# Kernel optimization log

Hardware: AMD Instinct MI355X
Metric: run time of the kernel (lower is better)

## Reference

```python
import jax, jax.numpy as jnp
import numpy as np

B, S, H = 4, 2048, 3072
NQ, NKV, D = 16, 8, 256
NEG = -2.3819763e38  # large negative for masking


def setup_inputs() -> dict:
    key = jax.random.key(0)
    ks = jax.random.split(key, 8)
    hidden_states = jax.random.normal(ks[0], (B, S, H), dtype=jnp.float32)
    # rotary frequencies: angle theta per (pos, dim-pair), Gemma-style base 10000
    inv_freq = 1.0 / (10000.0 ** (np.arange(0, D, 2, dtype=np.float32) / D))  # [D/2]
    t = np.arange(S, dtype=np.float32)
    ang = np.outer(t, inv_freq)  # [S, D/2]
    freqs_cos = jnp.broadcast_to(jnp.asarray(np.cos(ang)), (B, S, D // 2)).astype(jnp.float32)
    freqs_sin = jnp.broadcast_to(jnp.asarray(np.sin(ang)), (B, S, D // 2)).astype(jnp.float32)
    # additive causal mask [B,1,S,S]
    causal = jnp.tril(jnp.ones((S, S), dtype=bool))
    mask = jnp.where(causal, 0.0, NEG).astype(jnp.float32)[None, None]
    mask = jnp.broadcast_to(mask, (B, 1, S, S))
    sc = 0.02
    wq = jax.random.normal(ks[1], (NQ * D, H), dtype=jnp.float32) * sc
    wk = jax.random.normal(ks[2], (NKV * D, H), dtype=jnp.float32) * sc
    wv = jax.random.normal(ks[3], (NKV * D, H), dtype=jnp.float32) * sc
    wo = jax.random.normal(ks[4], (H, NQ * D), dtype=jnp.float32) * sc
    return {"hidden_states": hidden_states, "freqs_cos": freqs_cos,
            "freqs_sin": freqs_sin, "mask": mask,
            "wq": wq, "wk": wk, "wv": wv, "wo": wo}


def _apply_rotary(x, cos, sin):
    # x: [B,S,N,Dh]; cos/sin: [B,S,Dh/2]. Complex rotation: (x1 + i x2) * (cos + i sin)
    d2 = x.shape[-1] // 2
    x1, x2 = x[..., :d2], x[..., d2:]
    c = cos[:, :, None, :]
    s = sin[:, :, None, :]
    return jnp.concatenate([x1 * c - x2 * s, x1 * s + x2 * c], axis=-1)


def reference(hidden_states, freqs_cos, freqs_sin, mask, wq, wk, wv, wo):
    b, s, _ = hidden_states.shape
    scaling = D ** -0.5
    xq = (hidden_states @ wq.T).reshape(b, s, NQ, D)
    xk = (hidden_states @ wk.T).reshape(b, s, NKV, D)
    xv = (hidden_states @ wv.T).reshape(b, s, NKV, D)
    xq = _apply_rotary(xq, freqs_cos, freqs_sin)
    xk = _apply_rotary(xk, freqs_cos, freqs_sin)
    # GQA: repeat kv heads to match query heads
    g = NQ // NKV
    xk = jnp.repeat(xk, g, axis=2)  # [b,s,NQ,D]
    xv = jnp.repeat(xv, g, axis=2)
    scores = jnp.einsum('bqhd,bkhd->bhqk', xq * scaling, xk) + mask
    probs = jax.nn.softmax(scores, axis=-1)
    out = jnp.einsum('bhqk,bkhd->bqhd', probs, xv).reshape(b, s, NQ * D)
    return out @ wo.T
```

## Files before the change

kernel.cpp:

```cpp
#include <hip/hip_runtime.h>

#define DEVI __device__ __forceinline__

typedef __attribute__((ext_vector_type(8))) short s16x8;
typedef __attribute__((ext_vector_type(4))) float f32x4;
typedef unsigned short u16;

DEVI u16 f2bf(float f){
  unsigned u = __float_as_uint(f);
  u += 0x7FFFu + ((u >> 16) & 1u);
  return (u16)(u >> 16);
}
DEVI float bf2f(u16 s){ return __uint_as_float(((unsigned)s) << 16); }

DEVI void gload16(const void* g, void* l){
  __builtin_amdgcn_global_load_lds((const __attribute__((address_space(1))) void*)g,
                                   (__attribute__((address_space(3))) void*)l, 16, 0, 0);
}

__global__ __launch_bounds__(256) void cast_bf16_kernel(const float* __restrict__ src,
                                                        u16* __restrict__ dst, int n4){
  int i = blockIdx.x*256 + threadIdx.x;
  if (i < n4){
    float4 v = reinterpret_cast<const float4*>(src)[i];
    ushort4 o;
    o.x = f2bf(v.x); o.y = f2bf(v.y); o.z = f2bf(v.z); o.w = f2bf(v.w);
    reinterpret_cast<ushort4*>(dst)[i] = o;
  }
}

template<int MODE>
__global__ __launch_bounds__(512,2) void gemm8p_kernel(
    const u16* __restrict__ A, const u16* __restrict__ Bw,
    int K, int nbn, int Nn,
    const float* __restrict__ fc, const float* __restrict__ fs,
    float* __restrict__ Cf, u16* __restrict__ Qo, u16* __restrict__ Ko, u16* __restrict__ Vo)
{
  __shared__ u16 LDSb[2][32768];
  const int nwg = gridDim.x;
  const int bid0 = blockIdx.x;
  const int bid = (bid0 & 7)*(nwg >> 3) + (bid0 >> 3);
  const int bm = bid / nbn, bn = bid % nbn;
  const int t = threadIdx.x, ln = t&63;
  const int wvid = t>>6;
  const int wr = wvid>>2, wc = wvid&3;
  const int frow = ln&15, g = ln>>4;
  const int NT = K >> 6;

  size_t soff[2];
  #pragma unroll
  for (int i=0;i<2;i++){
    const int phys = (i*512 + t)*16;
    const int L = phys ^ (((phys>>7)&7)<<4);
    soff[i] = (size_t)(L >> 7) * K + ((L & 127) >> 1);
  }
  const u16* Apan = A  + (size_t)(bm*256)*K;
  const u16* Bpan = Bw + (size_t)(bn*256)*K;

  int aoff[8][2], boff[4][2];
  #pragma unroll
  for (int mi=0;mi<8;mi++){
    const int row = mi*16 + frow;
    #pragma unroll
    for (int ks=0;ks<2;ks++){
      const int L = row*128 + ks*64 + g*16;
      aoff[mi][ks] = wr*16384 + (L ^ ((row&7)<<4));
    }
  }
  #pragma unroll
  for (int ni=0;ni<4;ni++){
    const int row128 = wc*32 + (ni&1)*16 + frow;
    const int half   = ni>>1;
    #pragma unroll
    for (int ks=0;ks<2;ks++){
      const int L = row128*128 + ks*64 + g*16;
      boff[ni][ks] = 32768 + half*16384 + (L ^ ((row128&7)<<4));
    }
  }

  f32x4 acc[8][4];
  #pragma unroll
  for (int i=0;i<8;i++)
    #pragma unroll
    for (int j=0;j<4;j++) acc[i][j] = f32x4{0.f,0.f,0.f,0.f};

  auto stageHalf = [&](int buf, int ht, int tstep){
    char* dst = (char*)&LDSb[buf][0] + ht*16384;
    const u16* src = (ht < 2 ? Apan : Bpan) + (size_t)((ht&1)*128)*K + (size_t)tstep*64;
    #pragma unroll
    for (int i=0;i<2;i++)
      gload16(src + soff[i], dst + (i*512 + t)*16);
  };

  stageHalf(0,0,0); stageHalf(0,1,0); stageHalf(0,2,0); stageHalf(0,3,0);
  if (NT > 1){ stageHalf(1,2,1); stageHalf(1,3,1); }
  asm volatile("s_waitcnt vmcnt(4)" ::: "memory");
  __builtin_amdgcn_s_barrier();

  for (int T=0; T<NT; ++T){
    const char* sb = (const char*)&LDSb[T&1][0];
    s16x8 bh[4][2];
    #pragma unroll
    for (int p=0;p<4;++p){
      if (p==0){
        #pragma unroll
        for (int ni=0;ni<4;ni++)
          #pragma unroll
          for (int ks=0;ks<2;ks++)
            bh[ni][ks] = *(const s16x8*)(sb + boff[ni][ks]);
      }
      s16x8 afr[2][2];
      #pragma unroll
      for (int m2=0;m2<2;m2++)
        #pragma unroll
        for (int ks=0;ks<2;ks++)
          afr[m2][ks] = *(const s16x8*)(sb + aoff[p*2+m2][ks]);
      if      (p==0){ if (T+1 < NT) stageHalf((T+1)&1, 0, T+1); }
      else if (p==1){ if (T+1 < NT) stageHalf((T+1)&1, 1, T+1); }
      else if (p==2){ if (T+2 < NT) stageHalf(T&1,     2, T+2); }
      else          { if (T+2 < NT) stageHalf(T&1,     3, T+2); }
      __builtin_amdgcn_s_barrier();
      asm volatile("s_waitcnt lgkmcnt(0)" ::: "memory");
      __builtin_amdgcn_sched_barrier(0);
      __builtin_amdgcn_s_setprio(1);
      #pragma unroll
      for (int ks=0;ks<2;ks++)
        #pragma unroll
        for (int m2=0;m2<2;m2++)
          #pragma unroll
          for (int ni=0;ni<4;ni++)
            acc[p*2+m2][ni] = __builtin_amdgcn_mfma_f32_16x16x32_bf16(
                afr[m2][ks], bh[ni][ks], acc[p*2+m2][ni], 0,0,0);
      __builtin_amdgcn_s_setprio(0);
      __builtin_amdgcn_sched_barrier(0);
      if (p==3){
        if (T+2 < NT)       { asm volatile("s_waitcnt vmcnt(4)" ::: "memory"); }
        else if (T+2 == NT) { asm volatile("s_waitcnt vmcnt(0)" ::: "memory"); }
      }
      __builtin_amdgcn_s_barrier();
    }
  }

  const int mbase = bm*256 + wr*128;
  if (MODE == 0 && bn < 24){
    const bool isQ = (bn < 16);
    u16* dstB = isQ ? Qo : Ko;
    const int h  = isQ ? bn : (bn - 16);
    const int NH = isQ ? 16 : 8;
    #pragma unroll
    for (int mi=0;mi<8;mi++){
      #pragma unroll
      for (int ni=0;ni<2;ni++){
        const int dd = wc*32 + ni*16 + frow;
        #pragma unroll
        for (int r=0;r<4;r++){
          const int m = mbase + mi*16 + g*4 + r;
          const int b = m >> 11, s = m & 2047;
          const size_t ci = ((size_t)(b*2048 + s))*128 + dd;
          const float c  = fc[ci];
          const float sn = fs[ci];
          const float x1 = acc[mi][ni][r], x2 = acc[mi][ni+2][r];
          const size_t base = (((size_t)(b*NH + h)*2048 + s) << 8);
          dstB[base + dd]       = f2bf(x1*c - x2*sn);
          dstB[base + dd + 128] = f2bf(x1*sn + x2*c);
        }
      }
    }
  } else if (MODE == 0){
    u16* TB = (u16*)&LDSb[0][0];
    const int h  = bn - 24;
    const int b  = (bm*256) >> 11;
    const int s0 = (bm*256) & 2047;
    #pragma unroll
    for (int mi=0;mi<8;mi++){
      #pragma unroll
      for (int ni=0;ni<4;ni++){
        const int d  = wc*32 + (ni>>1)*128 + (ni&1)*16 + frow;
        const int sl = wr*128 + mi*16 + g*4;
        alignas(8) u16 p4[4];
        #pragma unroll
        for (int r=0;r<4;r++) p4[r] = f2bf(acc[mi][ni][r]);
        const int Tphys = (d*512 + sl*2) ^ ((d&7)<<4);
        *(uint2*)((char*)TB + Tphys) = *(const uint2*)p4;
      }
    }
    __syncthreads();
    #pragma unroll
    for (int i=0;i<16;i++){
      const int ci = i*512 + t;
      const int d = ci >> 5, sb2 = (ci & 31)*16;
      const int phys = (d*512 + sb2) ^ ((d&7)<<4);
      const s16x8 val = *(const s16x8*)((const char*)TB + phys);
      *(s16x8*)&Vo[(((size_t)(b*8 + h)*256 + d)*2048) + s0 + (sb2>>1)] = val;
    }
  } else {
    #pragma unroll
    for (int mi=0;mi<8;mi++){
      #pragma unroll
      for (int ni=0;ni<4;ni++){
        const int n = bn*256 + wc*32 + (ni>>1)*128 + (ni&1)*16 + frow;
        #pragma unroll
        for (int r=0;r<4;r++){
          const int m = mbase + mi*16 + g*4 + r;
          Cf[(size_t)m*Nn + n] = acc[mi][ni][r];
        }
      }
    }
  }
}

__global__ __launch_bounds__(512,2) void flash_attn_kernel(
    const u16* __restrict__ Qg, const u16* __restrict__ Kg,
    const u16* __restrict__ VTg, u16* __restrict__ Og)
{
  __shared__ u16 Kl[2][32*256];
  __shared__ u16 Vt[2][256*32];
  __shared__ u16 Pl[8][16*40];
  const int xb = blockIdx.x;
  const int kvh = blockIdx.y, b = blockIdx.z;
  const int t = threadIdx.x, wvid = t>>6, ln = t&63;
  const int frow = ln&15, g = ln>>4;
  const int qh = kvh*2 + (wvid>>2);
  const u16* Qp = Qg  + ((size_t)(b*16 + qh) << 19);
  const u16* Kp = Kg  + ((size_t)(b*8 + kvh) << 19);
  const u16* Vp = VTg + ((size_t)(b*8 + kvh) << 19);

  s16x8 ones;
  #pragma unroll
  for (int j=0;j<8;j++) ones[j] = (short)0x3F80;

  int kge[2]; int vrow[2]; int vcb[2];
  #pragma unroll
  for (int i=0;i<2;i++){
    const int ci = i*512 + t;
    kge[i] = (ci*8) ^ ((((unsigned)ci>>5)&7)<<3);
    const int phys = ci*16;
    const int L = phys ^ (((phys>>6)&3)<<4);
    vrow[i] = L >> 6;  vcb[i] = (L & 63) >> 1;
  }

  auto stageKV = [&](int kbase, int buf){
    #pragma unroll
    for (int i=0;i<2;i++){
      const int ci = i*512 + t;
      gload16(Kp + (size_t)kbase*256 + kge[i], &Kl[buf][(ci & ~63)*8]);
    }
    #pragma unroll
    for (int i=0;i<2;i++){
      const int ci = i*512 + t;
      gload16(Vp + (size_t)vrow[i]*2048 + kbase + vcb[i], &Vt[buf][(ci & ~63)*8]);
    }
  };

  #pragma unroll 1
  for (int seg=0; seg<2; seg++){
    const int qb = seg ? (31 - xb) : xb;
    const int q0 = qb*64 + (wvid&3)*16;
    const int ntiles = qb*2 + 2;

    s16x8 aq[8];
    #pragma unroll
    for (int kk=0;kk<8;kk++){
      s16x8 v = *(const s16x8*)&Qp[(size_t)(q0+frow)*256 + kk*32 + g*8];
      #pragma unroll
      for (int j=0;j<8;j++) v[j] = (short)f2bf(bf2f((u16)v[j]) * 0.0625f);
      aq[kk] = v;
    }

    f32x4 accO[16];
    #pragma unroll
    for (int i=0;i<16;i++) accO[i] = f32x4{0.f,0.f,0.f,0.f};
    f32x4 accL = f32x4{0.f,0.f,0.f,0.f};

    stageKV(0, 0);
    __syncthreads();

    for (int kt=0; kt<ntiles; kt++){
      const int kbase = kt*32;
      if (kt+1 < ntiles) stageKV(kbase + 32, (kt+1)&1);

      if (kbase <= q0 + 15){
        const char* Kb8 = (const char*)&Kl[kt&1][0];
        f32x4 sc[2];
        sc[0] = f32x4{0.f,0.f,0.f,0.f};
        sc[1] = f32x4{0.f,0.f,0.f,0.f};
        #pragma unroll
        for (int kb=0;kb<2;kb++){
          const int rr = kb*16 + frow;
          const int sw = (rr&7)<<4;
          const int bb = rr*512 + g*16;
          #pragma unroll
          for (int kk=0;kk<8;kk++){
            const s16x8 bk = *(const s16x8*)(Kb8 + ((bb + kk*64) ^ sw));
            sc[kb] = __builtin_amdgcn_mfma_f32_16x16x32_bf16(aq[kk], bk, sc[kb], 0,0,0);
          }
        }
        if (kbase + 31 > q0){
          #pragma unroll
          for (int r=0;r<4;r++){
            const int qrow = q0 + g*4 + r;
            if (kbase + frow > qrow)      sc[0][r] = -1e30f;
            if (kbase + 16 + frow > qrow) sc[1][r] = -1e30f;
          }
        }
        #pragma unroll
        for (int r=0;r<4;r++){
          const float p0 = __expf(fminf(sc[0][r], 30.f) - 8.f);
          const float p1 = __expf(fminf(sc[1][r], 30.f) - 8.f);
          Pl[wvid][(g*4+r)*40 + frow]      = f2bf(p0);
          Pl[wvid][(g*4+r)*40 + 16 + frow] = f2bf(p1);
        }
        asm volatile("s_waitcnt lgkmcnt(0)" ::: "memory");
        __builtin_amdgcn_sched_barrier(0);
        const s16x8 pf = *(const s16x8*)&Pl[wvid][frow*40 + g*8];
        accL = __builtin_amdgcn_mfma_f32_16x16x32_bf16(pf, ones, accL, 0,0,0);
        const char* Vb8 = (const char*)&Vt[kt&1][0];
        #pragma unroll
        for (int nb=0;nb<16;nb++){
          const int row = nb*16 + frow;
          const s16x8 vf = *(const s16x8*)(Vb8 + ((row*64 + g*16) ^ ((row&3)<<4)));
          accO[nb] = __builtin_amdgcn_mfma_f32_16x16x32_bf16(pf, vf, accO[nb], 0,0,0);
        }
      }

      __syncthreads();
    }

    f32x4 rl;
    #pragma unroll
    for (int r=0;r<4;r++) rl[r] = 1.0f / accL[r];
    #pragma unroll
    for (int nb=0;nb<16;nb++)
      #pragma unroll
      for (int r=0;r<4;r++){
        const int qrow = q0 + g*4 + r;
        Og[(((size_t)(b*2048 + qrow)*16 + qh) << 8) + nb*16 + frow] = f2bf(accO[nb][r] * rl[r]);
      }
  }
}

extern "C" void kernel_launch(void* const* d_in, const int* in_sizes, int n_in,
                              void* d_out, int out_size, void* d_ws, size_t ws_size,
                              hipStream_t stream) {
  const float* hidden = (const float*)d_in[0];
  const float* fcos   = (const float*)d_in[1];
  const float* fsin   = (const float*)d_in[2];
  const float* wq = (const float*)d_in[4];
  const float* wk = (const float*)d_in[5];
  const float* wv = (const float*)d_in[6];
  const float* wo = (const float*)d_in[7];
  float* out = (float*)d_out;

  char* ws = (char*)d_ws;
  u16* Xb   = (u16*)(ws);
  u16* Wcat = (u16*)(ws + 50331648);
  u16* Wob  = (u16*)(ws + 100663296);
  u16* Qb   = (u16*)(ws + 125829120);
  u16* Kb   = (u16*)(ws + 192937984);
  u16* VTb  = (u16*)(ws + 226492416);
  u16* AOb  = (u16*)(ws + 260046848);

  cast_bf16_kernel<<<24576, 256, 0, stream>>>(hidden, Xb, 6291456);
  cast_bf16_kernel<<<12288, 256, 0, stream>>>(wq, Wcat,              3145728);
  cast_bf16_kernel<<< 6144, 256, 0, stream>>>(wk, Wcat + 12582912,   1572864);
  cast_bf16_kernel<<< 6144, 256, 0, stream>>>(wv, Wcat + 18874368,   1572864);
  cast_bf16_kernel<<<12288, 256, 0, stream>>>(wo, Wob,               3145728);

  gemm8p_kernel<0><<<32*32, 512, 0, stream>>>(Xb, Wcat, 3072, 32, 8192,
                                              fcos, fsin, nullptr, Qb, Kb, VTb);

  flash_attn_kernel<<<dim3(16,8,4), 512, 0, stream>>>(Qb, Kb, VTb, AOb);

  gemm8p_kernel<1><<<32*12, 512, 0, stream>>>(AOb, Wob, 4096, 12, 3072,
                                              nullptr, nullptr, out, nullptr, nullptr, nullptr);
}
```

Before: 937.1 us.

## Fuse weight/input casts into one kernel and halve M-tile for output GEMM

Replaces five separate fp32-to-bf16 cast launches with a single grid-stride kernel that routes each index to the right source and destination. It also templates the GEMM on the M tile size and runs the output projection with 128-row tiles instead of 256, doubling its workgroup count from 384 to 768. The smaller tile is meant to fill the GPU's compute units better on the small output GEMM, at the cost of lower per-workgroup reuse of B tiles. The QKV GEMM keeps the original tile.

```diff
diff --git a/kernel.cpp b/kernel.cpp
--- a/kernel.cpp
+++ b/kernel.cpp
@@ -18,25 +18,39 @@
                                    (__attribute__((address_space(3))) void*)l, 16, 0, 0);
 }
 
-__global__ __launch_bounds__(256) void cast_bf16_kernel(const float* __restrict__ src,
-                                                        u16* __restrict__ dst, int n4){
-  int i = blockIdx.x*256 + threadIdx.x;
-  if (i < n4){
-    float4 v = reinterpret_cast<const float4*>(src)[i];
+__global__ __launch_bounds__(256) void cast_all_kernel(
+    const float* __restrict__ h,  const float* __restrict__ wq,
+    const float* __restrict__ wk, const float* __restrict__ wv,
+    const float* __restrict__ wo,
+    u16* __restrict__ Xb, u16* __restrict__ Wcat, u16* __restrict__ Wob)
+{
+  const int total = 15728640;
+  for (int i = blockIdx.x*256 + threadIdx.x; i < total; i += gridDim.x*256){
+    const float* src; u16* dst; int off;
+    if (i < 6291456)      { src = h;  dst = Xb;              off = i; }
+    else if (i < 9437184) { src = wq; dst = Wcat;            off = i - 6291456; }
+    else if (i < 11010048){ src = wk; dst = Wcat + 12582912; off = i - 9437184; }
+    else if (i < 12582912){ src = wv; dst = Wcat + 18874368; off = i - 11010048; }
+    else                  { src = wo; dst = Wob;             off = i - 12582912; }
+    float4 v = reinterpret_cast<const float4*>(src)[off];
     ushort4 o;
     o.x = f2bf(v.x); o.y = f2bf(v.y); o.z = f2bf(v.z); o.w = f2bf(v.w);
-    reinterpret_cast<ushort4*>(dst)[i] = o;
-  }
-}
-
-template<int MODE>
+    reinterpret_cast<ushort4*>(dst)[off] = o;
+  }
+}
+
+template<int MODE, int MI>
 __global__ __launch_bounds__(512,2) void gemm8p_kernel(
     const u16* __restrict__ A, const u16* __restrict__ Bw,
     int K, int nbn, int Nn,
     const float* __restrict__ fc, const float* __restrict__ fs,
     float* __restrict__ Cf, u16* __restrict__ Qo, u16* __restrict__ Ko, u16* __restrict__ Vo)
 {
-  __shared__ u16 LDSb[2][32768];
+  constexpr int AH   = MI*2048;
+  constexpr int BOFF = 2*AH;
+  constexpr int ACH  = MI/4;
+  constexpr int APH  = MI/4;
+  __shared__ u16 LDSb[2][(BOFF + 32768)/2];
   const int nwg = gridDim.x;
   const int bid0 = blockIdx.x;
   const int bid = (bid0 & 7)*(nwg >> 3) + (bid0 >> 3);
@@ -47,24 +61,30 @@
   const int frow = ln&15, g = ln>>4;
   const int NT = K >> 6;
 
-  size_t soff[2];
+  size_t soffA[ACH], soffB[2];
+  #pragma unroll
+  for (int i=0;i<ACH;i++){
+    const int phys = (i*512 + t)*16;
+    const int L = phys ^ (((phys>>7)&7)<<4);
+    soffA[i] = (size_t)(L >> 7) * K + ((L & 127) >> 1);
+  }
   #pragma unroll
   for (int i=0;i<2;i++){
     const int phys = (i*512 + t)*16;
     const int L = phys ^ (((phys>>7)&7)<<4);
-    soff[i] = (size_t)(L >> 7) * K + ((L & 127) >> 1);
-  }
-  const u16* Apan = A  + (size_t)(bm*256)*K;
+    soffB[i] = (size_t)(L >> 7) * K + ((L & 127) >> 1);
+  }
+  const u16* Apan = A  + (size_t)(bm*(MI*32))*K;
   const u16* Bpan = Bw + (size_t)(bn*256)*K;
 
-  int aoff[8][2], boff[4][2];
-  #pragma unroll
-  for (int mi=0;mi<8;mi++){
+  int aoff[MI][2], boff[4][2];
+  #pragma unroll
+  for (int mi=0;mi<MI;mi++){
     const int row = mi*16 + frow;
     #pragma unroll
     for (int ks=0;ks<2;ks++){
       const int L = row*128 + ks*64 + g*16;
-      aoff[mi][ks] = wr*16384 + (L ^ ((row&7)<<4));
+      aoff[mi][ks] = wr*AH + (L ^ ((row&7)<<4));
     }
   }
   #pragma unroll
@@ -74,22 +94,30 @@
     #pragma unroll
     for (int ks=0;ks<2;ks++){
       const int L = row128*128 + ks*64 + g*16;
-      boff[ni][ks] = 32768 + half*16384 + (L ^ ((row128&7)<<4));
-    }
-  }
-
-  f32x4 acc[8][4];
-  #pragma unroll
-  for (int i=0;i<8;i++)
+      boff[ni][ks] = BOFF + half*16384 + (L ^ ((row128&7)<<4));
+    }
+  }
+
+  f32x4 acc[MI][4];
+  #pragma unroll
+  for (int i=0;i<MI;i++)
     #pragma unroll
     for (int j=0;j<4;j++) acc[i][j] = f32x4{0.f,0.f,0.f,0.f};
 
   auto stageHalf = [&](int buf, int ht, int tstep){
-    char* dst = (char*)&LDSb[buf][0] + ht*16384;
-    const u16* src = (ht < 2 ? Apan : Bpan) + (size_t)((ht&1)*128)*K + (size_t)tstep*64;
-    #pragma unroll
-    for (int i=0;i<2;i++)
-      gload16(src + soff[i], dst + (i*512 + t)*16);
+    if (ht < 2){
+      char* dst = (char*)&LDSb[buf][0] + ht*AH;
+      const u16* src = Apan + (size_t)(ht*(MI*16))*K + (size_t)tstep*64;
+      #pragma unroll
+      for (int i=0;i<ACH;i++)
+        gload16(src + soffA[i], dst + (i*512 + t)*16);
+    } else {
+      char* dst = (char*)&LDSb[buf][0] + BOFF + (ht-2)*16384;
+      const u16* src = Bpan + (size_t)((ht&1)*128)*K + (size_t)tstep*64;
+      #pragma unroll
+      for (int i=0;i<2;i++)
+        gload16(src + soffB[i], dst + (i*512 + t)*16);
+    }
   };
 
   stageHalf(0,0,0); stageHalf(0,1,0); stageHalf(0,2,0); stageHalf(0,3,0);
@@ -109,12 +137,12 @@
           for (int ks=0;ks<2;ks++)
             bh[ni][ks] = *(const s16x8*)(sb + boff[ni][ks]);
       }
-      s16x8 afr[2][2];
-      #pragma unroll
-      for (int m2=0;m2<2;m2++)
+      s16x8 afr[APH][2];
+      #pragma unroll
+      for (int j=0;j<APH;j++)
         #pragma unroll
         for (int ks=0;ks<2;ks++)
-          afr[m2][ks] = *(const s16x8*)(sb + aoff[p*2+m2][ks]);
+          afr[j][ks] = *(const s16x8*)(sb + aoff[p*APH+j][ks]);
       if      (p==0){ if (T+1 < NT) stageHalf((T+1)&1, 0, T+1); }
       else if (p==1){ if (T+1 < NT) stageHalf((T+1)&1, 1, T+1); }
       else if (p==2){ if (T+2 < NT) stageHalf(T&1,     2, T+2); }
@@ -126,11 +154,11 @@
       #pragma unroll
       for (int ks=0;ks<2;ks++)
         #pragma unroll
-        for (int m2=0;m2<2;m2++)
+        for (int j=0;j<APH;j++)
           #pragma unroll
           for (int ni=0;ni<4;ni++)
-            acc[p*2+m2][ni] = __builtin_amdgcn_mfma_f32_16x16x32_bf16(
-                afr[m2][ks], bh[ni][ks], acc[p*2+m2][ni], 0,0,0);
+            acc[p*APH+j][ni] = __builtin_amdgcn_mfma_f32_16x16x32_bf16(
+                afr[j][ks], bh[ni][ks], acc[p*APH+j][ni], 0,0,0);
       __builtin_amdgcn_s_setprio(0);
       __builtin_amdgcn_sched_barrier(0);
       if (p==3){
@@ -141,14 +169,14 @@
     }
   }
 
-  const int mbase = bm*256 + wr*128;
+  const int mbase = bm*(MI*32) + wr*(MI*16);
   if (MODE == 0 && bn < 24){
     const bool isQ = (bn < 16);
     u16* dstB = isQ ? Qo : Ko;
     const int h  = isQ ? bn : (bn - 16);
     const int NH = isQ ? 16 : 8;
     #pragma unroll
-    for (int mi=0;mi<8;mi++){
+    for (int mi=0;mi<MI;mi++){
       #pragma unroll
       for (int ni=0;ni<2;ni++){
         const int dd = wc*32 + ni*16 + frow;
@@ -172,11 +200,11 @@
     const int b  = (bm*256) >> 11;
     const int s0 = (bm*256) & 2047;
     #pragma unroll
-    for (int mi=0;mi<8;mi++){
+    for (int mi=0;mi<MI;mi++){
       #pragma unroll
       for (int ni=0;ni<4;ni++){
         const int d  = wc*32 + (ni>>1)*128 + (ni&1)*16 + frow;
-        const int sl = wr*128 + mi*16 + g*4;
+        const int sl = wr*(MI*16) + mi*16 + g*4;
         alignas(8) u16 p4[4];
         #pragma unroll
         for (int r=0;r<4;r++) p4[r] = f2bf(acc[mi][ni][r]);
@@ -195,7 +223,7 @@
     }
   } else {
     #pragma unroll
-    for (int mi=0;mi<8;mi++){
+    for (int mi=0;mi<MI;mi++){
       #pragma unroll
       for (int ni=0;ni<4;ni++){
         const int n = bn*256 + wc*32 + (ni>>1)*128 + (ni&1)*16 + frow;
@@ -360,17 +388,13 @@
   u16* VTb  = (u16*)(ws + 226492416);
   u16* AOb  = (u16*)(ws + 260046848);
 
-  cast_bf16_kernel<<<24576, 256, 0, stream>>>(hidden, Xb, 6291456);
-  cast_bf16_kernel<<<12288, 256, 0, stream>>>(wq, Wcat,              3145728);
-  cast_bf16_kernel<<< 6144, 256, 0, stream>>>(wk, Wcat + 12582912,   1572864);
-  cast_bf16_kernel<<< 6144, 256, 0, stream>>>(wv, Wcat + 18874368,   1572864);
-  cast_bf16_kernel<<<12288, 256, 0, stream>>>(wo, Wob,               3145728);
-
-  gemm8p_kernel<0><<<32*32, 512, 0, stream>>>(Xb, Wcat, 3072, 32, 8192,
-                                              fcos, fsin, nullptr, Qb, Kb, VTb);
+  cast_all_kernel<<<4096, 256, 0, stream>>>(hidden, wq, wk, wv, wo, Xb, Wcat, Wob);
+
+  gemm8p_kernel<0,8><<<32*32, 512, 0, stream>>>(Xb, Wcat, 3072, 32, 8192,
+                                                fcos, fsin, nullptr, Qb, Kb, VTb);
 
   flash_attn_kernel<<<dim3(16,8,4), 512, 0, stream>>>(Qb, Kb, VTb, AOb);
 
-  gemm8p_kernel<1><<<32*12, 512, 0, stream>>>(AOb, Wob, 4096, 12, 3072,
-                                              nullptr, nullptr, out, nullptr, nullptr, nullptr);
-}
+  gemm8p_kernel<1,4><<<64*12, 512, 0, stream>>>(AOb, Wob, 4096, 12, 3072,
+                                                nullptr, nullptr, out, nullptr, nullptr, nullptr);
+}
```

New measurement: 933.5 us. Within noise of the previous version (-0.4%).
